# Performance work log

Hardware: AMD Instinct MI355X
Metric: run time of the kernel (lower is better)

The kernel has to match this reference:

```python
import jax, jax.numpy as jnp
import numpy as np

N = 100000   # nodes
E = 640000   # edges
F = 128      # num_features
H = 128      # hidden_channels
EPS = 1e-5   # BatchNorm1d eps
SCALE = 0.05


def setup_inputs() -> dict:
    key = jax.random.key(0)
    ks = jax.random.split(key, 16)
    inp = {
        "x": jax.random.normal(ks[0], (N, F), dtype=jnp.float32),
        "edge_index": jax.random.randint(ks[1], (2, E), 0, N, dtype=jnp.int32),
    }
    dims = [(F, H), (H, H), (H, H)]
    k = 2
    for i, (din, dout) in enumerate(dims):
        inp[f"Wl{i}"] = jax.random.normal(ks[k], (dout, din), dtype=jnp.float32) * SCALE
        inp[f"bl{i}"] = jax.random.normal(ks[k + 1], (dout,), dtype=jnp.float32) * SCALE
        inp[f"Wr{i}"] = jax.random.normal(ks[k + 2], (dout, din), dtype=jnp.float32) * SCALE
        k += 3
    inp["W1"] = jax.random.normal(ks[k], (H, H), dtype=jnp.float32) * SCALE
    inp["b1"] = jax.random.normal(ks[k + 1], (H,), dtype=jnp.float32) * SCALE
    inp["W2"] = jax.random.normal(ks[k + 2], (2, H), dtype=jnp.float32) * SCALE
    inp["b2"] = jax.random.normal(ks[k + 3], (2,), dtype=jnp.float32) * SCALE
    return inp


def _batchnorm(x):
    # BatchNorm1d(track_running_stats=False, affine=False): biased batch stats
    mu = jnp.mean(x, axis=0)
    var = jnp.var(x, axis=0)
    return (x - mu) / jnp.sqrt(var + EPS)


def _sage_conv(x, src, dst, Wl, bl, Wr):
    # PyG SAGEConv (aggr='mean'): out = lin_l(mean_agg(x[src] -> dst)) + lin_r(x)
    msg = x[src]                                             # [E, din]
    ssum = jax.ops.segment_sum(msg, dst, num_segments=N)     # [N, din]
    cnt = jax.ops.segment_sum(jnp.ones((E,), x.dtype), dst, num_segments=N)
    agg = ssum / jnp.maximum(cnt, 1.0)[:, None]              # mean, 0 for isolated
    return agg @ Wl.T + bl + x @ Wr.T


def reference(x, edge_index, Wl0, bl0, Wr0, Wl1, bl1, Wr1, Wl2, bl2, Wr2, W1, b1, W2, b2):
    src, dst = edge_index[0], edge_index[1]
    for Wl, bl, Wr in ((Wl0, bl0, Wr0), (Wl1, bl1, Wr1), (Wl2, bl2, Wr2)):
        x = jax.nn.relu(_batchnorm(_sage_conv(x, src, dst, Wl, bl, Wr)))
    x = jax.nn.relu(_batchnorm(x @ W1.T + b1))
    return x @ W2.T + b2
```

## Files before the change

kernel.cpp:

```cpp
#include <hip/hip_runtime.h>
#include <stdint.h>

typedef __bf16 v8bf __attribute__((ext_vector_type(8)));
typedef float f32x4 __attribute__((ext_vector_type(4)));
typedef float f32x2 __attribute__((ext_vector_type(2)));

__device__ __forceinline__ float b2f(unsigned short u) {
    unsigned int x = ((unsigned int)u) << 16;
    return __builtin_bit_cast(float, x);
}
__device__ __forceinline__ float b2f_lo(unsigned int v) {
    return __builtin_bit_cast(float, v << 16);
}
__device__ __forceinline__ float b2f_hi(unsigned int v) {
    return __builtin_bit_cast(float, v & 0xffff0000u);
}
__device__ __forceinline__ unsigned short f2b(float f) {
    unsigned int x = __builtin_bit_cast(unsigned int, f);
    unsigned int r = (x + 0x7fffu + ((x >> 16) & 1u)) >> 16;
    return (unsigned short)r;
}

__device__ __forceinline__ void load_lds16(const void* g, void* l) {
    __builtin_amdgcn_global_load_lds(
        (__attribute__((address_space(1))) void*)(const void*)g,
        (__attribute__((address_space(3))) void*)l, 16, 0, 0);
}

__device__ __forceinline__ void barrier_raw() {
    __builtin_amdgcn_sched_barrier(0);
    __builtin_amdgcn_s_barrier();
    __builtin_amdgcn_sched_barrier(0);
}

#define VMW(n) asm volatile("s_waitcnt vmcnt(" #n ")" ::: "memory")

struct WSrc { const float* p[7]; const float* s[6]; };

__global__ void k_prologue(WSrc w, unsigned short* __restrict__ wbuf,
                           const int* __restrict__ src, const int* __restrict__ dst,
                           int* __restrict__ pos, int* __restrict__ csr, int E,
                           const float* __restrict__ x, unsigned short* __restrict__ xcat,
                           unsigned short* __restrict__ y,
                           int n, int nFill, int nCvtw, int nCopyx) {
    int bid = blockIdx.x;
    int t = threadIdx.x;
    if (bid < nFill) {
        int i4 = (bid * 256 + t) * 4;
        if (((E & 3) == 0) && i4 < E) {
            int4 d4 = *(const int4*)&dst[i4];
            int4 s4 = *(const int4*)&src[i4];
            int p;
            p = atomicAdd(&pos[d4.x], 1); if (p < 64) csr[((size_t)d4.x << 6) + p] = s4.x;
            p = atomicAdd(&pos[d4.y], 1); if (p < 64) csr[((size_t)d4.y << 6) + p] = s4.y;
            p = atomicAdd(&pos[d4.z], 1); if (p < 64) csr[((size_t)d4.z << 6) + p] = s4.z;
            p = atomicAdd(&pos[d4.w], 1); if (p < 64) csr[((size_t)d4.w << 6) + p] = s4.w;
        } else {
            for (int i = i4; i < min(i4 + 4, E); i++) {
                int d = dst[i];
                int p = atomicAdd(&pos[d], 1);
                if (p < 64) csr[((size_t)d << 6) + p] = src[i];
            }
        }
    } else if (bid < nFill + nCvtw) {
        int idx = (bid - nFill) * 256 + t;
        if (idx < 115458) {
            float v;
            if (idx < 114688) {
                v = w.p[idx >> 14][idx & 16383];
            } else {
                int rem = idx - 114688;
                int tt, j;
                if (rem < 512)      { tt = rem >> 7; j = rem & 127; }
                else if (rem < 768) { tt = 4; j = rem - 512; }
                else                { tt = 5; j = rem - 768; }
                v = w.s[tt][j];
            }
            wbuf[idx] = f2b(v);
        } else if (idx < 115458 + 64) {
            int k = idx - 115458;
            if (k < 32) {
                ushort4 z; z.x = z.y = z.z = z.w = 0;
                *(ushort4*)&xcat[(size_t)n * 256 + 128 + k * 4] = z;
            } else {
                ushort4 m; m.x = m.y = m.z = m.w = 0xFF7Fu;
                *(ushort4*)&y[(size_t)n * 128 + (k - 32) * 4] = m;
            }
        }
    } else {
        int T = nCopyx * 256;
        int tid = (bid - nFill - nCvtw) * 256 + t;
        int total = n * 32;
        for (int i0 = tid; i0 < total; i0 += 4 * T) {
#pragma unroll
            for (int u = 0; u < 4; u++) {
                int i = i0 + u * T;
                if (i < total) {
                    int row = i >> 5, c4 = (i & 31) * 4;
                    float4 v = *(const float4*)&x[(size_t)row * 128 + c4];
                    ushort4 o;
                    o.x = f2b(v.x); o.y = f2b(v.y); o.z = f2b(v.z); o.w = f2b(v.w);
                    *(ushort4*)&xcat[(size_t)row * 256 + 128 + c4] = o;
                }
            }
        }
    }
}

__global__ void k_hist(const int* __restrict__ pos, int* __restrict__ hist, int n) {
    __shared__ int lh[32];
    int t = threadIdx.x;
    int i = blockIdx.x * 256 + t;
    if (t < 32) lh[t] = 0;
    __syncthreads();
    if (i < n) atomicAdd(&lh[31 - min(pos[i], 31)], 1);
    __syncthreads();
    if (t < 32) atomicAdd(&hist[t], lh[t]);
}

__global__ void k_order(const int* __restrict__ cnt, const int* __restrict__ hist,
                        int* __restrict__ binpos, int* __restrict__ order, int n) {
    __shared__ int lh[32], gb[32], hloc[32];
    int t = threadIdx.x;
    if (t < 32) { lh[t] = 0; hloc[t] = hist[t]; }
    __syncthreads();
    int i = blockIdx.x * 256 + t;
    int b = 0, r = 0;
    if (i < n) {
        b = 31 - min(cnt[i], 31);
        r = atomicAdd(&lh[b], 1);
    }
    __syncthreads();
    if (t < 32) {
        int off = 0;
        for (int k = 0; k < t; k++) off += hloc[k];
        gb[t] = off + atomicAdd(&binpos[t], lh[t]);
    }
    __syncthreads();
    if (i < n) order[gb[b] + r] = i;
}

__global__ __launch_bounds__(256) void k_agg(const unsigned short* __restrict__ xcat,
                                             const int* __restrict__ cnt, const int* __restrict__ csr,
                                             const int* __restrict__ order,
                                             unsigned short* __restrict__ outL, int n) {
    int t = threadIdx.x;
    int l = t & 15;
    int gbase = (t & 63) & ~15;
    int oi = blockIdx.x * 16 + (t >> 4);
    if (oi >= n) return;
    int d = order[oi];
    size_t s = (size_t)d << 6;
    int deg = cnt[d];
    f32x2 ax[4] = {};
    for (int base = 0; base < deg; base += 16) {
        int myidx = (base + l < deg) ? csr[s + base + l] : n;
        int lim = min(16, deg - base);
        for (int b = 0; b < lim; b += 8) {
            int idx[8];
            uint4 v[8];
#pragma unroll
            for (int u = 0; u < 8; u++) idx[u] = __shfl(myidx, gbase + b + u, 64);
#pragma unroll
            for (int u = 0; u < 8; u++)
                v[u] = *(const uint4*)(xcat + (((unsigned)idx[u]) << 8) + 128u + (unsigned)(l << 3));
#pragma unroll
            for (int u = 0; u < 8; u++) {
                unsigned int uu[4] = {v[u].x, v[u].y, v[u].z, v[u].w};
#pragma unroll
                for (int k = 0; k < 4; k++) {
                    f32x2 tv;
                    tv.x = b2f_lo(uu[k]);
                    tv.y = b2f_hi(uu[k]);
                    ax[k] += tv;
                }
            }
        }
    }
    float ic = 1.0f / (float)max(deg, 1);
    uint4 o;
    unsigned int* op = (unsigned int*)&o;
#pragma unroll
    for (int k = 0; k < 4; k++)
        op[k] = ((unsigned int)f2b(ax[k].y * ic) << 16) | f2b(ax[k].x * ic);
    *(uint4*)&outL[(size_t)d * 256 + l * 8] = o;
}

__global__ __launch_bounds__(256) void k_aggbn(const unsigned short* __restrict__ Y,
                                               const float* __restrict__ statp,
                                               const int* __restrict__ cnt, const int* __restrict__ csr,
                                               const int* __restrict__ order,
                                               unsigned short* __restrict__ xcat, int n, float invN) {
    __shared__ float smu[128], sinv[128], sq[128];
    int t = threadIdx.x;
    if (t < 128) {
        float s = 0.f;
#pragma unroll
        for (int sl = 0; sl < 32; sl++) s += statp[sl * 256 + t];
        smu[t] = s * invN;
    } else {
        int u = t - 128;
        float q = 0.f;
#pragma unroll
        for (int sl = 0; sl < 32; sl++) q += statp[sl * 256 + 128 + u];
        sq[u] = q;
    }
    __syncthreads();
    if (t < 128) {
        float mu = smu[t];
        sinv[t] = rsqrtf(sq[t] * invN - mu * mu + 1e-5f);
    }
    __syncthreads();
    int l = t & 15;
    int gbase = (t & 63) & ~15;
    int oi = blockIdx.x * 16 + (t >> 4);
    if (oi >= n) return;
    int d = order[oi];
    f32x2 mu2[4];
    float iv[8];
#pragma unroll
    for (int k = 0; k < 4; k++) {
        mu2[k].x = smu[l * 8 + 2 * k];
        mu2[k].y = smu[l * 8 + 2 * k + 1];
    }
#pragma unroll
    for (int k = 0; k < 8; k++) iv[k] = sinv[l * 8 + k];
    {
        uint4 vo = *(const uint4*)&Y[(size_t)oi * 128 + l * 8];
        unsigned int uu[4] = {vo.x, vo.y, vo.z, vo.w};
        uint4 o;
        unsigned int* op = (unsigned int*)&o;
#pragma unroll
        for (int k = 0; k < 4; k++) {
            float a = fmaxf((b2f_lo(uu[k]) - mu2[k].x) * iv[2 * k], 0.f);
            float b = fmaxf((b2f_hi(uu[k]) - mu2[k].y) * iv[2 * k + 1], 0.f);
            op[k] = ((unsigned int)f2b(b) << 16) | f2b(a);
        }
        *(uint4*)&xcat[(size_t)oi * 256 + 128 + l * 8] = o;
    }
    size_t s = (size_t)d << 6;
    int deg = cnt[d];
    f32x2 z2 = {0.f, 0.f};
    f32x2 ax[4] = {};
    for (int base = 0; base < deg; base += 16) {
        int myidx = (base + l < deg) ? csr[s + base + l] : n;
        int lim = min(16, deg - base);
        for (int b = 0; b < lim; b += 8) {
            int idx[8];
            uint4 v[8];
#pragma unroll
            for (int u = 0; u < 8; u++) idx[u] = __shfl(myidx, gbase + b + u, 64);
#pragma unroll
            for (int u = 0; u < 8; u++)
                v[u] = *(const uint4*)(Y + (((unsigned)idx[u]) << 7) + (unsigned)(l << 3));
#pragma unroll
            for (int u = 0; u < 8; u++) {
                unsigned int uu[4] = {v[u].x, v[u].y, v[u].z, v[u].w};
#pragma unroll
                for (int k = 0; k < 4; k++) {
                    f32x2 tv;
                    tv.x = b2f_lo(uu[k]);
                    tv.y = b2f_hi(uu[k]);
                    tv = tv - mu2[k];
                    tv = __builtin_elementwise_max(tv, z2);
                    ax[k] += tv;
                }
            }
        }
    }
    float ic = 1.0f / (float)max(deg, 1);
    uint4 o;
    unsigned int* op = (unsigned int*)&o;
#pragma unroll
    for (int k = 0; k < 4; k++)
        op[k] = ((unsigned int)f2b(ax[k].y * (iv[2 * k + 1] * ic)) << 16)
              | f2b(ax[k].x * (iv[2 * k] * ic));
    *(uint4*)&xcat[(size_t)d * 256 + l * 8] = o;
}

template<int NCH>
__global__ __launch_bounds__(256) void k_wgemm(const unsigned short* __restrict__ A, int lda, int aoff,
                                               const unsigned short* __restrict__ W0,
                                               const unsigned short* __restrict__ W1,
                                               const unsigned short* __restrict__ bias,
                                               unsigned short* __restrict__ Y,
                                               float* __restrict__ statp, int nrows) {
    constexpr int HALF = NCH / 2;
    constexpr int LPH = HALF / 2;
    __shared__ __align__(16) unsigned short Ws[NCH][4096];
    __shared__ __align__(16) unsigned short As[2][HALF][1024];
    int t = threadIdx.x;
    int wv = t >> 6, lane = t & 63;
    int quad = lane >> 4, l16 = lane & 15;

    for (int c = 0; c < NCH; c++) {
        const unsigned short* Wp = (c < 4) ? W0 : W1;
        int wkc = (c & 3) * 32;
#pragma unroll
        for (int q = 0; q < 2; q++) {
            int r = q * 64 + (t >> 2);
            load_lds16(Wp + (size_t)r * 128 + wkc + (t & 3) * 8,
                       &Ws[c][(size_t)r * 32 + (t & 3) * 8]);
        }
    }

    float bn[2][4];
#pragma unroll
    for (int j = 0; j < 2; j++) {
        int c0 = wv * 32 + j * 16 + quad * 4;
        uint2 bu = *(const uint2*)&bias[c0];
        bn[j][0] = b2f_lo(bu.x); bn[j][1] = b2f_hi(bu.x);
        bn[j][2] = b2f_lo(bu.y); bn[j][3] = b2f_hi(bu.y);
    }

    f32x4 cs_[2] = {}, cq_[2] = {};

    int ntiles = (nrows + 31) >> 5;
    int tt = t & 127;
    int half = t >> 7;
    int ar = tt >> 2, ac = (tt & 3) * 8;

    auto stage = [&](int m0, int hb, int buf) {
#pragma unroll
        for (int p2 = 0; p2 < LPH; p2++) {
            int slot = p2 * 2 + half;
            int gr = m0 + ar;
            if (gr >= nrows) gr = nrows - 1;
            load_lds16(A + (size_t)gr * lda + aoff + (hb + slot) * 32 + ac,
                       &As[buf][slot][(size_t)ar * 32 + ac]);
        }
    };
    auto compute_half = [&](int hb, int buf, f32x4 (&acc)[2][2]) {
#pragma unroll
        for (int c = 0; c < HALF; c++) {
            v8bf af[2], bfv[2];
#pragma unroll
            for (int i = 0; i < 2; i++)
                af[i] = *(const v8bf*)&As[buf][c][(i * 16 + l16) * 32 + quad * 8];
#pragma unroll
            for (int j = 0; j < 2; j++)
                bfv[j] = *(const v8bf*)&Ws[hb + c][(wv * 32 + j * 16 + l16) * 32 + quad * 8];
#pragma unroll
            for (int i = 0; i < 2; i++)
#pragma unroll
                for (int j = 0; j < 2; j++)
                    acc[i][j] = __builtin_amdgcn_mfma_f32_16x16x32_bf16(bfv[j], af[i], acc[i][j], 0, 0, 0);
        }
    };

    int mt = blockIdx.x;
    stage(mt * 32, 0, 0);
    stage(mt * 32, HALF, 1);
    bool first = true;
    for (; mt < ntiles; mt += (int)gridDim.x) {
        int m0 = mt * 32;
        int nxt = mt + (int)gridDim.x;
        int nm0 = (nxt < ntiles) ? nxt * 32 : m0;

        if (first) {
            if constexpr (LPH == 2) VMW(2); else VMW(1);
        } else {
            if constexpr (LPH == 2) VMW(6); else VMW(5);
        }
        barrier_raw();

        f32x4 acc[2][2] = {};
        compute_half(0, 0, acc);
        barrier_raw();
        stage(nm0, 0, 0);

        if constexpr (LPH == 2) VMW(2); else VMW(1);
        barrier_raw();
        compute_half(HALF, 1, acc);

#pragma unroll
        for (int i = 0; i < 2; i++)
#pragma unroll
            for (int j = 0; j < 2; j++)
#pragma unroll
                for (int u = 0; u < 4; u++)
                    acc[i][j][u] += bn[j][u];
#pragma unroll
        for (int i = 0; i < 2; i++) {
            int row = m0 + i * 16 + l16;
            int srow = (row < nrows) ? row : (nrows + 1);
#pragma unroll
            for (int j = 0; j < 2; j++) {
                int c0 = wv * 32 + j * 16 + quad * 4;
                uint2 o;
                o.x = ((unsigned int)f2b(acc[i][j][1]) << 16) | f2b(acc[i][j][0]);
                o.y = ((unsigned int)f2b(acc[i][j][3]) << 16) | f2b(acc[i][j][2]);
                *(uint2*)&Y[(size_t)srow * 128 + c0] = o;
            }
        }
#pragma unroll
        for (int i = 0; i < 2; i++) {
            int row = m0 + i * 16 + l16;
            if (row < nrows) {
#pragma unroll
                for (int j = 0; j < 2; j++)
#pragma unroll
                    for (int u = 0; u < 4; u++) {
                        float v = acc[i][j][u];
                        cs_[j][u] += v;
                        cq_[j][u] += v * v;
                    }
            }
        }
        barrier_raw();
        stage(nm0, HALF, 1);
        first = false;
    }

    float* sp = statp + (blockIdx.x & 31) * 256;
#pragma unroll
    for (int j = 0; j < 2; j++) {
        for (int m = 1; m < 16; m <<= 1) {
#pragma unroll
            for (int u = 0; u < 4; u++) {
                cs_[j][u] += __shfl_xor(cs_[j][u], m, 64);
                cq_[j][u] += __shfl_xor(cq_[j][u], m, 64);
            }
        }
        if (l16 == 0) {
            int c0 = wv * 32 + j * 16 + quad * 4;
#pragma unroll
            for (int u = 0; u < 4; u++) {
                atomicAdd(&sp[c0 + u], cs_[j][u]);
                atomicAdd(&sp[128 + c0 + u], cq_[j][u]);
            }
        }
    }
}

__global__ __launch_bounds__(256) void k_bnrelu(const unsigned short* __restrict__ Y,
                                                const float* __restrict__ statp,
                                                unsigned short* __restrict__ out, int ldo,
                                                int n, float invN) {
    __shared__ float smu[128], sinv[128], sq[128];
    int t = threadIdx.x;
    if (t < 128) {
        float s = 0.f;
#pragma unroll
        for (int sl = 0; sl < 32; sl++) s += statp[sl * 256 + t];
        smu[t] = s * invN;
    } else {
        int u = t - 128;
        float q = 0.f;
#pragma unroll
        for (int sl = 0; sl < 32; sl++) q += statp[sl * 256 + 128 + u];
        sq[u] = q;
    }
    __syncthreads();
    if (t < 128) {
        float mu = smu[t];
        sinv[t] = rsqrtf(sq[t] * invN - mu * mu + 1e-5f);
    }
    __syncthreads();
    int i = blockIdx.x * 256 + t;
    if (i >= n * 16) return;
    int row = i >> 4, f8 = (i & 15) * 8;
    uint4 v = *(const uint4*)&Y[(size_t)row * 128 + f8];
    unsigned int u[4] = {v.x, v.y, v.z, v.w};
    uint4 o;
    unsigned int* op = (unsigned int*)&o;
    for (int k = 0; k < 4; k++) {
        int f = f8 + k * 2;
        float a = fmaxf((b2f_lo(u[k]) - smu[f]) * sinv[f], 0.f);
        float b = fmaxf((b2f_hi(u[k]) - smu[f + 1]) * sinv[f + 1], 0.f);
        op[k] = ((unsigned int)f2b(b) << 16) | f2b(a);
    }
    *(uint4*)&out[(size_t)row * ldo + f8] = o;
}

__global__ __launch_bounds__(256) void k_bnfinal(const unsigned short* __restrict__ Y,
                                                 const float* __restrict__ statp,
                                                 const unsigned short* __restrict__ W2,
                                                 const unsigned short* __restrict__ b2v,
                                                 float* __restrict__ out, int n, float invN) {
    __shared__ float smu[128], sinv[128], sq[128];
    int t = threadIdx.x;
    if (t < 128) {
        float s = 0.f;
#pragma unroll
        for (int sl = 0; sl < 32; sl++) s += statp[sl * 256 + t];
        smu[t] = s * invN;
    } else {
        int u = t - 128;
        float q = 0.f;
#pragma unroll
        for (int sl = 0; sl < 32; sl++) q += statp[sl * 256 + 128 + u];
        sq[u] = q;
    }
    __syncthreads();
    if (t < 128) {
        float mu = smu[t];
        sinv[t] = rsqrtf(sq[t] * invN - mu * mu + 1e-5f);
    }
    __syncthreads();
    int wid = t >> 6, lane = t & 63;
    int r = blockIdx.x * 4 + wid;
    if (r >= n) return;
    int f2 = lane * 2;
    unsigned int v = *(const unsigned int*)&Y[(size_t)r * 128 + f2];
    float a = fmaxf((b2f_lo(v) - smu[f2]) * sinv[f2], 0.f);
    float b = fmaxf((b2f_hi(v) - smu[f2 + 1]) * sinv[f2 + 1], 0.f);
    unsigned int w0 = *(const unsigned int*)&W2[f2];
    unsigned int w1 = *(const unsigned int*)&W2[128 + f2];
    float d0 = a * b2f_lo(w0) + b * b2f_hi(w0);
    float d1 = a * b2f_lo(w1) + b * b2f_hi(w1);
    for (int o = 32; o > 0; o >>= 1) {
        d0 += __shfl_down(d0, o, 64);
        d1 += __shfl_down(d1, o, 64);
    }
    if (lane == 0) {
        float2 o2;
        o2.x = d0 + b2f(b2v[0]);
        o2.y = d1 + b2f(b2v[1]);
        *(float2*)&out[(size_t)r * 2] = o2;
    }
}

extern "C" void kernel_launch(void* const* d_in, const int* in_sizes, int n_in,
                              void* d_out, int out_size, void* d_ws, size_t ws_size,
                              hipStream_t stream) {
    const int N = in_sizes[0] / 128;
    const int E = in_sizes[1] / 2;

    const float* x = (const float*)d_in[0];
    const int* ei = (const int*)d_in[1];
    const int* srcp = ei;
    const int* dstp = ei + E;
    float* out = (float*)d_out;

    char* w = (char*)d_ws;
    auto align256 = [](size_t v) { return (v + 255) & ~(size_t)255; };
    size_t o_xcat = 0;
    size_t o_y    = align256(o_xcat + (size_t)(N + 1) * 256 * 2);
    size_t o_csr  = align256(o_y + (size_t)(N + 2) * 128 * 2);
    size_t o_ord  = align256(o_csr + (size_t)N * 64 * 4);
    size_t o_wbuf = align256(o_ord + (size_t)N * 4);
    size_t o_pos  = align256(o_wbuf + 115712 * 2);
    size_t o_stat = o_pos + (size_t)N * 4;
    size_t o_hist = o_stat + 4 * 8192 * 4;
    size_t o_binp = o_hist + 32 * 4;

    unsigned short* xcat = (unsigned short*)(w + o_xcat);
    unsigned short* y    = (unsigned short*)(w + o_y);
    int* csr = (int*)(w + o_csr);
    int* ord  = (int*)(w + o_ord);
    unsigned short* wbuf = (unsigned short*)(w + o_wbuf);
    int* pos = (int*)(w + o_pos);
    float* stat = (float*)(w + o_stat);
    int* hist = (int*)(w + o_hist);
    int* binp = (int*)(w + o_binp);

    const unsigned short* Wl[3] = {wbuf + 0,      wbuf + 32768, wbuf + 65536};
    const unsigned short* Wr[3] = {wbuf + 16384,  wbuf + 49152, wbuf + 81920};
    const unsigned short* W1b   = wbuf + 98304;
    const unsigned short* bl[3] = {wbuf + 114688, wbuf + 114816, wbuf + 114944};
    const unsigned short* b1b   = wbuf + 115072;
    const unsigned short* W2b   = wbuf + 115200;
    const unsigned short* b2b   = wbuf + 115456;

    WSrc wsrc;
    wsrc.p[0] = (const float*)d_in[2];
    wsrc.p[1] = (const float*)d_in[4];
    wsrc.p[2] = (const float*)d_in[5];
    wsrc.p[3] = (const float*)d_in[7];
    wsrc.p[4] = (const float*)d_in[8];
    wsrc.p[5] = (const float*)d_in[10];
    wsrc.p[6] = (const float*)d_in[11];
    wsrc.s[0] = (const float*)d_in[3];
    wsrc.s[1] = (const float*)d_in[6];
    wsrc.s[2] = (const float*)d_in[9];
    wsrc.s[3] = (const float*)d_in[12];
    wsrc.s[4] = (const float*)d_in[13];
    wsrc.s[5] = (const float*)d_in[14];

    const int NB = (N + 255) / 256;
    const int nFill = (E + 1023) / 1024;
    const int nCvtw = (115458 + 64 + 255) / 256;
    const int nCopyx = 1024;

    hipMemsetAsync(w + o_pos, 0, (size_t)N * 4 + 4 * 8192 * 4 + 64 * 4, stream);

    k_prologue<<<nFill + nCvtw + nCopyx, 256, 0, stream>>>(wsrc, wbuf, srcp, dstp, pos, csr, E,
                                                           x, xcat, y, N, nFill, nCvtw, nCopyx);
    k_hist<<<NB, 256, 0, stream>>>(pos, hist, N);
    k_order<<<NB, 256, 0, stream>>>(pos, hist, binp, ord, N);

    const int wg_grid = 512;
    const int agg16_grid = (N + 15) / 16;
    const int wave_grid = (N + 3) / 4;
    const int bnr_grid = (N * 16 + 255) / 256;
    const float invN = 1.0f / (float)N;

    k_agg<<<agg16_grid, 256, 0, stream>>>(xcat, pos, csr, ord, xcat, N);
    k_wgemm<8><<<wg_grid, 256, 0, stream>>>(xcat, 256, 0, Wl[0], Wr[0], bl[0], y, stat + 0 * 8192, N);
    for (int i = 1; i < 3; i++) {
        k_aggbn<<<agg16_grid, 256, 0, stream>>>(y, stat + (i - 1) * 8192, pos, csr, ord, xcat, N, invN);
        k_wgemm<8><<<wg_grid, 256, 0, stream>>>(xcat, 256, 0, Wl[i], Wr[i], bl[i], y, stat + i * 8192, N);
    }
    k_bnrelu<<<bnr_grid, 256, 0, stream>>>(y, stat + 2 * 8192, xcat + 128, 256, N, invN);
    k_wgemm<4><<<wg_grid, 256, 0, stream>>>(xcat, 256, 128, W1b, W1b, b1b, y, stat + 3 * 8192, N);
    k_bnfinal<<<wave_grid, 256, 0, stream>>>(y, stat + 3 * 8192, W2b, b2b, out, N, invN);
}
```

Before: 400.8 us.

## Fuse final BatchNorm+ReLU into the W1 GEMM, and use one edge per thread in CSR fill

The standalone BN+ReLU pass after the third SAGE layer is removed. A new GEMM kernel applies the normalization and ReLU while staging each A tile into LDS, then runs the W1 matmul and accumulates the column statistics. This drops one full read and write of the N×128 bf16 intermediate and one kernel launch. The output is written in place over the input buffer, which relies on each block reading and writing only its own row tiles. Separately, the CSR fill now handles one edge per thread instead of four vectorized edges, which changes the atomic issue pattern.

```diff
diff --git a/kernel.cpp b/kernel.cpp
--- a/kernel.cpp
+++ b/kernel.cpp
@@ -46,21 +46,11 @@
     int bid = blockIdx.x;
     int t = threadIdx.x;
     if (bid < nFill) {
-        int i4 = (bid * 256 + t) * 4;
-        if (((E & 3) == 0) && i4 < E) {
-            int4 d4 = *(const int4*)&dst[i4];
-            int4 s4 = *(const int4*)&src[i4];
-            int p;
-            p = atomicAdd(&pos[d4.x], 1); if (p < 64) csr[((size_t)d4.x << 6) + p] = s4.x;
-            p = atomicAdd(&pos[d4.y], 1); if (p < 64) csr[((size_t)d4.y << 6) + p] = s4.y;
-            p = atomicAdd(&pos[d4.z], 1); if (p < 64) csr[((size_t)d4.z << 6) + p] = s4.z;
-            p = atomicAdd(&pos[d4.w], 1); if (p < 64) csr[((size_t)d4.w << 6) + p] = s4.w;
-        } else {
-            for (int i = i4; i < min(i4 + 4, E); i++) {
-                int d = dst[i];
-                int p = atomicAdd(&pos[d], 1);
-                if (p < 64) csr[((size_t)d << 6) + p] = src[i];
-            }
+        int i = bid * 256 + t;
+        if (i < E) {
+            int d = dst[i];
+            int p = atomicAdd(&pos[d], 1);
+            if (p < 64) csr[((size_t)d << 6) + p] = src[i];
         }
     } else if (bid < nFill + nCvtw) {
         int idx = (bid - nFill) * 256 + t;
@@ -433,12 +423,30 @@
     }
 }
 
-__global__ __launch_bounds__(256) void k_bnrelu(const unsigned short* __restrict__ Y,
-                                                const float* __restrict__ statp,
-                                                unsigned short* __restrict__ out, int ldo,
-                                                int n, float invN) {
+__global__ __launch_bounds__(256) void k_wgemm_bn(const unsigned short* __restrict__ A,
+                                                  const float* __restrict__ statp,
+                                                  const unsigned short* __restrict__ W0,
+                                                  const unsigned short* __restrict__ bias,
+                                                  unsigned short* __restrict__ Y,
+                                                  float* __restrict__ statp_out,
+                                                  int nrows, float invN) {
+    __shared__ __align__(16) unsigned short Ws[4][4096];
+    __shared__ __align__(16) unsigned short As[4][1024];
     __shared__ float smu[128], sinv[128], sq[128];
     int t = threadIdx.x;
+    int wv = t >> 6, lane = t & 63;
+    int quad = lane >> 4, l16 = lane & 15;
+
+    for (int c = 0; c < 4; c++) {
+        int wkc = c * 32;
+#pragma unroll
+        for (int q = 0; q < 2; q++) {
+            int r = q * 64 + (t >> 2);
+            load_lds16(W0 + (size_t)r * 128 + wkc + (t & 3) * 8,
+                       &Ws[c][(size_t)r * 32 + (t & 3) * 8]);
+        }
+    }
+
     if (t < 128) {
         float s = 0.f;
 #pragma unroll
@@ -457,20 +465,136 @@
         sinv[t] = rsqrtf(sq[t] * invN - mu * mu + 1e-5f);
     }
     __syncthreads();
-    int i = blockIdx.x * 256 + t;
-    if (i >= n * 16) return;
-    int row = i >> 4, f8 = (i & 15) * 8;
-    uint4 v = *(const uint4*)&Y[(size_t)row * 128 + f8];
-    unsigned int u[4] = {v.x, v.y, v.z, v.w};
-    uint4 o;
-    unsigned int* op = (unsigned int*)&o;
-    for (int k = 0; k < 4; k++) {
-        int f = f8 + k * 2;
-        float a = fmaxf((b2f_lo(u[k]) - smu[f]) * sinv[f], 0.f);
-        float b = fmaxf((b2f_hi(u[k]) - smu[f + 1]) * sinv[f + 1], 0.f);
-        op[k] = ((unsigned int)f2b(b) << 16) | f2b(a);
-    }
-    *(uint4*)&out[(size_t)row * ldo + f8] = o;
+
+    int c16 = (t & 15) * 8;
+    int sch = (t & 15) >> 2;
+    int sac = (t & 3) * 8;
+    int sr = t >> 4;
+    float mu8[8], iv8[8];
+#pragma unroll
+    for (int k = 0; k < 8; k++) { mu8[k] = smu[c16 + k]; iv8[k] = sinv[c16 + k]; }
+
+    float bn[2][4];
+#pragma unroll
+    for (int j = 0; j < 2; j++) {
+        int c0 = wv * 32 + j * 16 + quad * 4;
+        uint2 bu = *(const uint2*)&bias[c0];
+        bn[j][0] = b2f_lo(bu.x); bn[j][1] = b2f_hi(bu.x);
+        bn[j][2] = b2f_lo(bu.y); bn[j][3] = b2f_hi(bu.y);
+    }
+
+    f32x4 cs_[2] = {}, cq_[2] = {};
+
+    int ntiles = (nrows + 31) >> 5;
+    int mt = blockIdx.x;
+    uint4 ra0, ra1;
+    {
+        int g0 = min(mt * 32 + sr, nrows - 1);
+        int g1 = min(mt * 32 + 16 + sr, nrows - 1);
+        ra0 = *(const uint4*)(A + (size_t)g0 * 128 + c16);
+        ra1 = *(const uint4*)(A + (size_t)g1 * 128 + c16);
+    }
+    auto xf = [&](uint4 v) -> uint4 {
+        unsigned int uu[4] = {v.x, v.y, v.z, v.w};
+        uint4 o; unsigned int* op = (unsigned int*)&o;
+#pragma unroll
+        for (int k = 0; k < 4; k++) {
+            float a = fmaxf((b2f_lo(uu[k]) - mu8[2 * k]) * iv8[2 * k], 0.f);
+            float b = fmaxf((b2f_hi(uu[k]) - mu8[2 * k + 1]) * iv8[2 * k + 1], 0.f);
+            op[k] = ((unsigned int)f2b(b) << 16) | f2b(a);
+        }
+        return o;
+    };
+
+    for (; mt < ntiles; mt += (int)gridDim.x) {
+        int m0 = mt * 32;
+        int nxt = mt + (int)gridDim.x;
+
+        VMW(0);
+        barrier_raw();
+        *(uint4*)&As[sch][(size_t)sr * 32 + sac] = xf(ra0);
+        *(uint4*)&As[sch][(size_t)(16 + sr) * 32 + sac] = xf(ra1);
+        __syncthreads();
+
+        if (nxt < ntiles) {
+            int g0 = min(nxt * 32 + sr, nrows - 1);
+            int g1 = min(nxt * 32 + 16 + sr, nrows - 1);
+            ra0 = *(const uint4*)(A + (size_t)g0 * 128 + c16);
+            ra1 = *(const uint4*)(A + (size_t)g1 * 128 + c16);
+        }
+
+        f32x4 acc[2][2] = {};
+#pragma unroll
+        for (int c = 0; c < 4; c++) {
+            v8bf af[2], bfv[2];
+#pragma unroll
+            for (int i = 0; i < 2; i++)
+                af[i] = *(const v8bf*)&As[c][(i * 16 + l16) * 32 + quad * 8];
+#pragma unroll
+            for (int j = 0; j < 2; j++)
+                bfv[j] = *(const v8bf*)&Ws[c][(wv * 32 + j * 16 + l16) * 32 + quad * 8];
+#pragma unroll
+            for (int i = 0; i < 2; i++)
+#pragma unroll
+                for (int j = 0; j < 2; j++)
+                    acc[i][j] = __builtin_amdgcn_mfma_f32_16x16x32_bf16(bfv[j], af[i], acc[i][j], 0, 0, 0);
+        }
+
+#pragma unroll
+        for (int i = 0; i < 2; i++)
+#pragma unroll
+            for (int j = 0; j < 2; j++)
+#pragma unroll
+                for (int u = 0; u < 4; u++)
+                    acc[i][j][u] += bn[j][u];
+#pragma unroll
+        for (int i = 0; i < 2; i++) {
+            int row = m0 + i * 16 + l16;
+            int srow = (row < nrows) ? row : (nrows + 1);
+#pragma unroll
+            for (int j = 0; j < 2; j++) {
+                int c0 = wv * 32 + j * 16 + quad * 4;
+                uint2 o;
+                o.x = ((unsigned int)f2b(acc[i][j][1]) << 16) | f2b(acc[i][j][0]);
+                o.y = ((unsigned int)f2b(acc[i][j][3]) << 16) | f2b(acc[i][j][2]);
+                *(uint2*)&Y[(size_t)srow * 128 + c0] = o;
+            }
+        }
+#pragma unroll
+        for (int i = 0; i < 2; i++) {
+            int row = m0 + i * 16 + l16;
+            if (row < nrows) {
+#pragma unroll
+                for (int j = 0; j < 2; j++)
+#pragma unroll
+                    for (int u = 0; u < 4; u++) {
+                        float v = acc[i][j][u];
+                        cs_[j][u] += v;
+                        cq_[j][u] += v * v;
+                    }
+            }
+        }
+    }
+
+    float* sp = statp_out + (blockIdx.x & 31) * 256;
+#pragma unroll
+    for (int j = 0; j < 2; j++) {
+        for (int m = 1; m < 16; m <<= 1) {
+#pragma unroll
+            for (int u = 0; u < 4; u++) {
+                cs_[j][u] += __shfl_xor(cs_[j][u], m, 64);
+                cq_[j][u] += __shfl_xor(cq_[j][u], m, 64);
+            }
+        }
+        if (l16 == 0) {
+            int c0 = wv * 32 + j * 16 + quad * 4;
+#pragma unroll
+            for (int u = 0; u < 4; u++) {
+                atomicAdd(&sp[c0 + u], cs_[j][u]);
+                atomicAdd(&sp[128 + c0 + u], cq_[j][u]);
+            }
+        }
+    }
 }
 
 __global__ __launch_bounds__(256) void k_bnfinal(const unsigned short* __restrict__ Y,
@@ -579,7 +703,7 @@
     wsrc.s[5] = (const float*)d_in[14];
 
     const int NB = (N + 255) / 256;
-    const int nFill = (E + 1023) / 1024;
+    const int nFill = (E + 255) / 256;
     const int nCvtw = (115458 + 64 + 255) / 256;
     const int nCopyx = 1024;
 
@@ -593,7 +717,6 @@
     const int wg_grid = 512;
     const int agg16_grid = (N + 15) / 16;
     const int wave_grid = (N + 3) / 4;
-    const int bnr_grid = (N * 16 + 255) / 256;
     const float invN = 1.0f / (float)N;
 
     k_agg<<<agg16_grid, 256, 0, stream>>>(xcat, pos, csr, ord, xcat, N);
@@ -602,7 +725,6 @@
         k_aggbn<<<agg16_grid, 256, 0, stream>>>(y, stat + (i - 1) * 8192, pos, csr, ord, xcat, N, invN);
         k_wgemm<8><<<wg_grid, 256, 0, stream>>>(xcat, 256, 0, Wl[i], Wr[i], bl[i], y, stat + i * 8192, N);
     }
-    k_bnrelu<<<bnr_grid, 256, 0, stream>>>(y, stat + 2 * 8192, xcat + 128, 256, N, invN);
-    k_wgemm<4><<<wg_grid, 256, 0, stream>>>(xcat, 256, 128, W1b, W1b, b1b, y, stat + 3 * 8192, N);
+    k_wgemm_bn<<<wg_grid, 256, 0, stream>>>(y, stat + 2 * 8192, W1b, b1b, y, stat + 3 * 8192, N, invN);
     k_bnfinal<<<wave_grid, 256, 0, stream>>>(y, stat + 3 * 8192, W2b, b2b, out, N, invN);
 }
```

Result: faster. 370.7 us (-7.5%).
